# Optimization experiments

Hardware: AMD Instinct MI355X
Metric: run time of the kernel (lower is better)

The kernel has to match this reference:

```python
import jax, jax.numpy as jnp
import numpy as np
from jax import lax

T, B, D, H, L, NDIR = 512, 64, 512, 512, 3, 2

def _lengths():
    return 512 - 4 * np.arange(64)  # per-sequence lengths, non-increasing

def _qdq(w):
    # simulate dynamic int8 symmetric per-tensor weight quantization
    s = jnp.max(jnp.abs(w)) / 127.0
    return jnp.clip(jnp.round(w / s), -127, 127) * s

def setup_inputs() -> dict:
    key = jax.random.key(0)
    ks = jax.random.split(key, 9)
    lengths = _lengths()
    bs = np.array([(lengths > t).sum() for t in range(T)], dtype=np.int64)  # [T]
    pack_idx = np.concatenate([t * B + np.arange(bs[t]) for t in range(T)]).astype(np.int32)
    sc = 0.05
    data = jax.random.normal(ks[0], (int(bs.sum()), D), jnp.float32)
    h0 = jax.random.normal(ks[1], (L * NDIR, B, H), jnp.float32)
    c0 = jax.random.normal(ks[2], (L * NDIR, B, H), jnp.float32)
    w_ih0 = _qdq(jax.random.normal(ks[3], (NDIR, 4 * H, D)) * sc)
    w_hh0 = _qdq(jax.random.normal(ks[4], (NDIR, 4 * H, H)) * sc)
    b0 = jax.random.normal(ks[5], (NDIR, 4 * H)) * sc  # b_ih + b_hh combined
    w_ih_r = _qdq(jax.random.normal(ks[6], (L - 1, NDIR, 4 * H, NDIR * H)) * sc)
    w_hh_r = _qdq(jax.random.normal(ks[7], (L - 1, NDIR, 4 * H, H)) * sc)
    b_r = jax.random.normal(ks[8], (L - 1, NDIR, 4 * H)) * sc
    return {"data": data, "h0": h0, "c0": c0, "w_ih0": w_ih0, "w_hh0": w_hh0, "b0": b0,
            "w_ih_r": w_ih_r, "w_hh_r": w_hh_r, "b_r": b_r,
            "batch_sizes": jnp.asarray(bs), "pack_idx": jnp.asarray(pack_idx)}

def _run_dir(x, mask, h0, c0, w_ih, w_hh, b):
    # x: [T,B,in], mask: [T,B]; batch the input GEMM over all timesteps
    gx = jnp.einsum('tbd,gd->tbg', x, w_ih) + b  # [T,B,4H]
    def step(carry, inp):
        h, c = carry
        gx_t, m = inp
        gates = gx_t + h @ w_hh.T
        i, f, g, o = jnp.split(gates, 4, axis=-1)  # PyTorch gate order i,f,g,o
        c_new = jax.nn.sigmoid(f) * c + jax.nn.sigmoid(i) * jnp.tanh(g)
        h_new = jax.nn.sigmoid(o) * jnp.tanh(c_new)
        m = m[:, None]
        return (jnp.where(m, h_new, h), jnp.where(m, c_new, c)), jnp.where(m, h_new, h)
    (hT, cT), ys = lax.scan(step, (h0, c0), (gx, mask))
    return ys * mask[:, :, None], hT, cT

def _lstm(data, h0, c0, w_ih0, w_hh0, b0, w_ih_r, w_hh_r, b_r, batch_sizes, pack_idx):
    mask = jnp.arange(B)[None, :] < batch_sizes[:, None]          # [T,B] valid slots
    lengths = jnp.sum(mask, axis=0)                                # [B]
    rev_idx = jnp.clip(lengths[None, :] - 1 - jnp.arange(T)[:, None], 0, T - 1)  # [T,B]
    barange = jnp.arange(B)[None, :]
    x = jnp.zeros((T * B, D), data.dtype).at[pack_idx].set(data).reshape(T, B, D)
    h_ns, c_ns = [], []
    for l in range(L):
        outs = []
        for d in range(NDIR):
            if l == 0:
                w_ih, w_hh, b = w_ih0[d], w_hh0[d], b0[d]
            else:
                w_ih, w_hh, b = w_ih_r[l - 1, d], w_hh_r[l - 1, d], b_r[l - 1, d]
            hi, ci = h0[NDIR * l + d], c0[NDIR * l + d]
            if d == 0:
                ys, hT, cT = _run_dir(x, mask, hi, ci, w_ih, w_hh, b)
            else:
                x_rev = x[rev_idx, barange]               # per-sequence reversal
                ys_r, hT, cT = _run_dir(x_rev, mask, hi, ci, w_ih, w_hh, b)
                ys = ys_r[rev_idx, barange] * mask[:, :, None]
            outs.append(ys); h_ns.append(hT); c_ns.append(cT)
        x = jnp.concatenate(outs, axis=-1)  # [T,B,2H] feeds next layer
    out = x.reshape(T * B, NDIR * H)[pack_idx]  # repack to [total_tokens, 2H]
    return out, jnp.stack(h_ns), jnp.stack(c_ns)

def reference(data, h0, c0, w_ih0, w_hh0, b0, w_ih_r, w_hh_r, b_r, batch_sizes, pack_idx):
    return _lstm(data, h0, c0, w_ih0, w_hh0, b0, w_ih_r, w_hh_r, b_r, batch_sizes, pack_idx)
```

## Files before the change

kernel.cpp:

```cpp
#include <hip/hip_runtime.h>
#include <cmath>

typedef _Float16 f16;
typedef _Float16 half8 __attribute__((ext_vector_type(8)));
typedef float floatx4 __attribute__((ext_vector_type(4)));
typedef unsigned u32x4 __attribute__((ext_vector_type(4)));

#define NT 512
#define NB 64
#define NH 512
#define NG 2048
#define CHUNK 128

__device__ inline float sigf(float x) { return 1.0f / (1.0f + __expf(-x)); }
__device__ inline float tanhfast(float x) { return 2.0f / (1.0f + __expf(-2.0f * x)) - 1.0f; }

__device__ inline void load_lds16(const f16* g, f16* l) {
  __builtin_amdgcn_global_load_lds(
      (__attribute__((address_space(1))) void*)g,
      (__attribute__((address_space(3))) void*)l, 16, 0, 0);
}

__global__ void prep_meta(const int* __restrict__ bs_raw, int* __restrict__ lens,
                          int* __restrict__ cum) {
  __shared__ int sbs[NT];
  int stride = (bs_raw[1] == 0) ? 2 : 1;
  for (int i = threadIdx.x; i < NT; i += 256) sbs[i] = bs_raw[i * stride];
  __syncthreads();
  for (int b = threadIdx.x; b < NB; b += 256) {
    int n = 0;
    for (int t = 0; t < NT; ++t) n += (sbs[t] > b);
    lens[b] = n;
  }
  if (threadIdx.x == 0) {
    int run = 0;
    for (int t = 0; t < NT; ++t) { cum[t] = run; run += sbs[t]; }
  }
}

__global__ void scatter_rows(const float* __restrict__ data, const int* __restrict__ pidx,
                             f16* __restrict__ X0) {
  int r = blockIdx.x;
  int row = pidx[r];
  const float* src = data + (size_t)r * 512;
  f16* dst = X0 + (size_t)row * 512;
  for (int k = threadIdx.x; k < 512; k += 256) dst[k] = (f16)src[k];
}

__global__ void f32_to_f16(const float* __restrict__ in, f16* __restrict__ out, size_t n) {
  size_t i = (size_t)blockIdx.x * 256 + threadIdx.x;
  size_t stride = (size_t)gridDim.x * 256;
  for (; i < n; i += stride) out[i] = (f16)in[i];
}

__global__ void init_h(const float* __restrict__ h0, const float* __restrict__ c0,
                       float* __restrict__ hsave, float* __restrict__ csave,
                       unsigned* __restrict__ ht, unsigned* __restrict__ ctr, int layer) {
  int idx = blockIdx.x * 256 + threadIdx.x;
  int d = idx >> 15, rem = idx & 32767;
  float hv = h0[(size_t)(2 * layer + d) * NB * NH + rem];
  float cv = c0[(size_t)(2 * layer + d) * NB * NH + rem];
  hsave[idx] = hv;
  csave[idx] = cv;
  union { f16 f; unsigned short s; } hc; hc.f = (f16)hv;
  unsigned word = ((unsigned)(layer * NT) << 16) | hc.s;
  __hip_atomic_store(ht + (size_t)d * NB * NH + rem, word,
                     __ATOMIC_RELAXED, __HIP_MEMORY_SCOPE_AGENT);
  if (blockIdx.x == 0) {
    __hip_atomic_store(ctr + threadIdx.x, (unsigned)(layer * NT),
                       __ATOMIC_RELAXED, __HIP_MEMORY_SCOPE_AGENT);
  }
}

__global__ __launch_bounds__(256) void gemm_gx(const f16* __restrict__ A,
                                               const f16* __restrict__ W,
                                               const float* __restrict__ bias,
                                               const int* __restrict__ lens,
                                               f16* __restrict__ gxc, int K, int c0) {
  const int d = blockIdx.z;
  const int m0 = blockIdx.y * 128;
  const int n0 = blockIdx.x * 128;
  const f16* Wd = W + (size_t)d * NG * K;

  __shared__ __align__(16) f16 As[128 * 32];
  __shared__ __align__(16) f16 Bs[128 * 32];

  const int tid = threadIdx.x, lane = tid & 63, wv = tid >> 6;
  const int wm = wv >> 1, wn = wv & 1;
  const int lrow = lane >> 2, lcol = (lane & 3) * 8;
  const int q = lane >> 4, nn = lane & 15;

  const f16* aptr[2];
  const f16* bptr[2];
#pragma unroll
  for (int i = 0; i < 2; ++i) {
    int ch = wv * 2 + i;
    int m = m0 + ch * 16 + lrow;
    int t = c0 + (m >> 6), b = m & 63;
    int tt = t;
    if (d) { tt = lens[b] - 1 - t; tt = tt < 0 ? 0 : (tt > NT - 1 ? NT - 1 : tt); }
    aptr[i] = A + (size_t)(tt * NB + b) * K + lcol;
    bptr[i] = Wd + (size_t)(n0 + ch * 16 + lrow) * K + lcol;
  }

  floatx4 acc[4][4] = {};
  for (int k0 = 0; k0 < K; k0 += 32) {
    __syncthreads();
#pragma unroll
    for (int i = 0; i < 2; ++i) {
      int ch = wv * 2 + i;
      load_lds16(aptr[i] + k0, As + ch * 512);
      load_lds16(bptr[i] + k0, Bs + ch * 512);
    }
    __syncthreads();
    half8 a[4], b[4];
#pragma unroll
    for (int f = 0; f < 4; ++f) {
      a[f] = *(const half8*)(As + (wm * 64 + f * 16 + nn) * 32 + q * 8);
      b[f] = *(const half8*)(Bs + (wn * 64 + f * 16 + nn) * 32 + q * 8);
    }
#pragma unroll
    for (int fm = 0; fm < 4; ++fm)
#pragma unroll
      for (int fn = 0; fn < 4; ++fn)
        acc[fm][fn] = __builtin_amdgcn_mfma_f32_16x16x32_f16(a[fm], b[fn], acc[fm][fn], 0, 0, 0);
  }

  f16* gxd = gxc + (size_t)d * CHUNK * NB * NG;
#pragma unroll
  for (int fn = 0; fn < 4; ++fn) {
    int col = n0 + wn * 64 + fn * 16 + nn;
    float bv = bias[d * NG + col];
#pragma unroll
    for (int fm = 0; fm < 4; ++fm) {
      int mb = m0 + wm * 64 + fm * 16 + q * 4;
#pragma unroll
      for (int r = 0; r < 4; ++r)
        gxd[(size_t)(mb + r) * NG + col] = (f16)(acc[fm][fn][r] + bv);
    }
  }
}

__global__ __launch_bounds__(256, 1) void lstm_rec(
    const f16* __restrict__ gxc, const f16* __restrict__ whh,
    const int* __restrict__ lens, const int* __restrict__ cum,
    float* __restrict__ hsave, float* __restrict__ csave,
    unsigned* __restrict__ ht, unsigned* __restrict__ ctr,
    f16* __restrict__ Y, float* __restrict__ outp,
    float* __restrict__ hT, float* __restrict__ cT,
    int c0, int mode, int layer) {
  const int tid = threadIdx.x, lane = tid & 63, wv = tid >> 6;
  const int g = blockIdx.x & 7, w = blockIdx.x >> 3;
  const int dir = g & 1, bsl = g >> 1;
  const int q = lane >> 4, nn = lane & 15;

  const int maxlen = lens[bsl * 16];
  int nst = maxlen - c0;
  if (nst <= 0) return;
  if (nst > CHUNK) nst = CHUNK;

  __shared__ __align__(16) unsigned As[2][16][260];
  __shared__ float s_g[4][16][17];

  const int jbase = w * 16 + wv * 4;
  const int coln = (nn >> 2) * NH + jbase + (nn & 3);
  const f16* whd = whh + (size_t)dir * NG * NH;
  half8 bf[16];
#pragma unroll
  for (int s = 0; s < 16; ++s) {
    bf[s] = *(const half8*)(whd + (size_t)coln * NH + s * 32 + q * 8);
    asm volatile("" : "+v"(bf[s]));
  }

  const int b_e = bsl * 16 + nn;
  const int jglob = jbase + q;
  const int lene = lens[b_e];
  const int brow = bsl * 16 + q * 4;
  const int lidx = (dir * NB + b_e) * NH + jglob;
  float h = hsave[lidx], c = csave[lidx];

  const f16* gxd = gxc + (size_t)dir * CHUNK * NB * NG;
  const int ebase = layer * NT;

  const unsigned* cslot = ctr + (size_t)g * 32 + (lane & 31);

  for (int ct = 0; ct < nst; ++ct) {
    const int t = c0 + ct;
    const int e = ebase + t;
    const int par = t & 1;

    float gxv[4];
#pragma unroll
    for (int r = 0; r < 4; ++r)
      gxv[r] = (float)gxd[(size_t)(ct * NB + brow + r) * NG + coln];

    {
      const unsigned* cp = cslot + par * 256;
      int it = 0;
      for (;;) {
        unsigned cv = __hip_atomic_load(cp, __ATOMIC_RELAXED, __HIP_MEMORY_SCOPE_AGENT);
        if (__ballot((int)cv >= e) == ~0ull) break;
        if (++it > 200000) break;
        __builtin_amdgcn_s_sleep(1);
      }
    }

    const unsigned long long* p64 =
        (const unsigned long long*)(ht + ((size_t)(par * 2 + dir) * NB + bsl * 16 + nn) * NH +
                                    wv * 128 + q * 8);
    unsigned long long wb[16];
    {
      int it = 0;
      for (;;) {
#pragma unroll
        for (int i = 0; i < 16; ++i)
          wb[i] = __hip_atomic_load(p64 + (i >> 2) * 16 + (i & 3), __ATOMIC_RELAXED,
                                    __HIP_MEMORY_SCOPE_AGENT);
        unsigned tg = 0xffffu;
#pragma unroll
        for (int i = 0; i < 16; ++i) {
          tg &= (unsigned)(wb[i] >> 16) & 0xffffu;
          tg &= (unsigned)(wb[i] >> 48);
        }
        if (__ballot(tg >= (unsigned)e) == ~0ull) break;
        if (++it > 50000) break;
        __builtin_amdgcn_s_sleep(1);
      }
    }

#pragma unroll
    for (int s = 0; s < 4; ++s) {
      unsigned d0 = (unsigned)(wb[4 * s + 0] & 0xffffu) | ((unsigned)(wb[4 * s + 0] >> 32) << 16);
      unsigned d1 = (unsigned)(wb[4 * s + 1] & 0xffffu) | ((unsigned)(wb[4 * s + 1] >> 32) << 16);
      unsigned d2 = (unsigned)(wb[4 * s + 2] & 0xffffu) | ((unsigned)(wb[4 * s + 2] >> 32) << 16);
      unsigned d3 = (unsigned)(wb[4 * s + 3] & 0xffffu) | ((unsigned)(wb[4 * s + 3] >> 32) << 16);
      *(u32x4*)&As[par][nn][wv * 64 + s * 16 + q * 4] = (u32x4){d0, d1, d2, d3};
    }
    __syncthreads();

    floatx4 acc0 = {0.f, 0.f, 0.f, 0.f}, acc1 = {0.f, 0.f, 0.f, 0.f};
#pragma unroll
    for (int s = 0; s < 8; ++s) {
      half8 a0 = *(const half8*)&As[par][nn][(2 * s) * 16 + q * 4];
      half8 a1 = *(const half8*)&As[par][nn][(2 * s + 1) * 16 + q * 4];
      acc0 = __builtin_amdgcn_mfma_f32_16x16x32_f16(a0, bf[2 * s], acc0, 0, 0, 0);
      acc1 = __builtin_amdgcn_mfma_f32_16x16x32_f16(a1, bf[2 * s + 1], acc1, 0, 0, 0);
    }
#pragma unroll
    for (int r4 = 0; r4 < 4; ++r4) s_g[wv][q * 4 + r4][nn] = acc0[r4] + acc1[r4] + gxv[r4];

    const bool act = (t < lene);
    if (act) {
      float gi = s_g[wv][nn][q];
      float gf = s_g[wv][nn][4 + q];
      float gg = s_g[wv][nn][8 + q];
      float go = s_g[wv][nn][12 + q];
      c = sigf(gf) * c + sigf(gi) * tanhfast(gg);
      h = sigf(go) * tanhfast(c);
    }
    union { f16 f; unsigned short s; } hc; hc.f = (f16)h;
    unsigned word = ((unsigned)(e + 1) << 16) | hc.s;
    __hip_atomic_store(ht + ((size_t)(((t + 1) & 1) * 2 + dir) * NB + b_e) * NH + jglob,
                       word, __ATOMIC_RELAXED, __HIP_MEMORY_SCOPE_AGENT);
    if (tid == 0)
      __hip_atomic_store(ctr + (size_t)(((t + 1) & 1) * 256 + g * 32 + w), (unsigned)(e + 1),
                         __ATOMIC_RELAXED, __HIP_MEMORY_SCOPE_AGENT);
    if (mode == 0) {
      int tp = act ? (dir ? (lene - 1 - t) : t) : t;
      Y[(size_t)(tp * NB + b_e) * (2 * NH) + dir * NH + jglob] = act ? (f16)h : (f16)0.f;
    } else if (act) {
      int tp = dir ? (lene - 1 - t) : t;
      outp[(size_t)(cum[tp] + b_e) * (2 * NH) + dir * NH + jglob] = h;
    }
  }

  hsave[lidx] = h;
  csave[lidx] = c;
  const int sidx = ((2 * layer + dir) * NB + b_e) * NH + jglob;
  hT[sidx] = h;
  cT[sidx] = c;
}

extern "C" void kernel_launch(void* const* d_in, const int* in_sizes, int n_in,
                              void* d_out, int out_size, void* d_ws, size_t ws_size,
                              hipStream_t stream) {
  const float* data  = (const float*)d_in[0];
  const float* h0    = (const float*)d_in[1];
  const float* c0    = (const float*)d_in[2];
  const float* w_ih0 = (const float*)d_in[3];
  const float* w_hh0 = (const float*)d_in[4];
  const float* b0    = (const float*)d_in[5];
  const float* w_ihr = (const float*)d_in[6];
  const float* w_hhr = (const float*)d_in[7];
  const float* b_r   = (const float*)d_in[8];
  const int* bs_raw  = (const int*)d_in[9];
  const int* pidx    = (const int*)d_in[10];
  const int nrows = in_sizes[0] / 512;
  float* out = (float*)d_out;

  f16* Y0 = (f16*)d_out;
  float* hT = out + (size_t)nrows * 1024;
  float* cT = hT + (size_t)6 * NB * NH;

  char* p = (char*)d_ws;
  auto take = [&](size_t bytes) {
    char* r = p;
    p += (bytes + 255) & ~(size_t)255;
    return (void*)r;
  };
  f16* gxc   = (f16*)take((size_t)2 * CHUNK * NB * NG * 2);
  f16* Y1    = (f16*)take((size_t)NT * NB * 1024 * 2);
  f16* X0    = Y1;
  f16* wih16 = (f16*)take((size_t)2 * NG * 1024 * 2);
  f16* whh16 = (f16*)take((size_t)2 * NG * NH * 2);
  unsigned* ht = (unsigned*)take((size_t)2 * 2 * NB * NH * 4);
  unsigned* ctr = (unsigned*)take((size_t)2 * 8 * 32 * 4);
  float* hsave = (float*)take((size_t)2 * NB * NH * 4);
  float* csave = (float*)take((size_t)2 * NB * NH * 4);
  int* lens = (int*)take(256);
  int* cum  = (int*)take(NT * 4);

  prep_meta<<<1, 256, 0, stream>>>(bs_raw, lens, cum);
  (void)hipMemsetAsync(X0, 0, (size_t)NT * NB * 512 * 2, stream);
  (void)hipMemsetAsync(ht, 0, (size_t)2 * 2 * NB * NH * 4, stream);
  (void)hipMemsetAsync(ctr, 0, (size_t)2 * 8 * 32 * 4, stream);
  scatter_rows<<<nrows, 256, 0, stream>>>(data, pidx, X0);

  for (int l = 0; l < 3; ++l) {
    const float* wih_f = (l == 0) ? w_ih0 : w_ihr + (size_t)(l - 1) * 2 * NG * 1024;
    const float* whh_f = (l == 0) ? w_hh0 : w_hhr + (size_t)(l - 1) * 2 * NG * NH;
    const float* bias  = (l == 0) ? b0 : b_r + (size_t)(l - 1) * 2 * NG;
    const int K = (l == 0) ? 512 : 1024;
    const f16* Xl = (l == 0) ? X0 : ((l == 1) ? Y0 : Y1);
    f16* Yl = (l == 0) ? Y0 : Y1;
    f32_to_f16<<<256, 256, 0, stream>>>(wih_f, wih16, (size_t)2 * NG * K);
    f32_to_f16<<<256, 256, 0, stream>>>(whh_f, whh16, (size_t)2 * NG * NH);
    init_h<<<256, 256, 0, stream>>>(h0, c0, hsave, csave, ht, ctr, l);
    for (int c = 0; c < 4; ++c) {
      gemm_gx<<<dim3(16, 64, 2), 256, 0, stream>>>(Xl, wih16, bias, lens, gxc, K, c * CHUNK);
      lstm_rec<<<256, 256, 0, stream>>>(gxc, whh16, lens, cum, hsave, csave, ht, ctr, Yl,
                                        out, hT, cT, c * CHUNK, (l == 2) ? 1 : 0, l);
    }
  }
}
```

Baseline: 7.056 ms.

## Overlap next-chunk input GEMM with recurrent kernel via double-buffered gate buffers

Extracts the input-projection GEMM into a device function and launches it inside the recurrent kernel as extra blocks (index 256 and up), computing the next chunk's gate pre-activations into a second buffer while the current chunk's recurrence runs. Double buffering is enabled only when the workspace has room for the second buffer. This hides the separate GEMM launches behind the latency-bound recurrence. The risk is that the extra blocks compete with the persistent recurrent blocks for CUs and bandwidth, or delay their scheduling, since those blocks spin-wait on each other.

```diff
diff --git a/kernel.cpp b/kernel.cpp
--- a/kernel.cpp
+++ b/kernel.cpp
@@ -72,14 +72,12 @@
   }
 }
 
-__global__ __launch_bounds__(256) void gemm_gx(const f16* __restrict__ A,
-                                               const f16* __restrict__ W,
-                                               const float* __restrict__ bias,
-                                               const int* __restrict__ lens,
-                                               f16* __restrict__ gxc, int K, int c0) {
-  const int d = blockIdx.z;
-  const int m0 = blockIdx.y * 128;
-  const int n0 = blockIdx.x * 128;
+__device__ void gemm_body(const f16* __restrict__ A, const f16* __restrict__ W,
+                          const float* __restrict__ bias, const int* __restrict__ lens,
+                          f16* __restrict__ gxc, int K, int c0, int id) {
+  const int d = id >> 10;
+  const int m0 = ((id >> 4) & 63) * 128;
+  const int n0 = (id & 15) * 128;
   const f16* Wd = W + (size_t)d * NG * K;
 
   __shared__ __align__(16) f16 As[128 * 32];
@@ -141,6 +139,15 @@
   }
 }
 
+__global__ __launch_bounds__(256) void gemm_gx(const f16* __restrict__ A,
+                                               const f16* __restrict__ W,
+                                               const float* __restrict__ bias,
+                                               const int* __restrict__ lens,
+                                               f16* __restrict__ gxc, int K, int c0) {
+  gemm_body(A, W, bias, lens, gxc, K, c0,
+            (int)(blockIdx.z * 1024 + blockIdx.y * 16 + blockIdx.x));
+}
+
 __global__ __launch_bounds__(256, 1) void lstm_rec(
     const f16* __restrict__ gxc, const f16* __restrict__ whh,
     const int* __restrict__ lens, const int* __restrict__ cum,
@@ -148,7 +155,13 @@
     unsigned* __restrict__ ht, unsigned* __restrict__ ctr,
     f16* __restrict__ Y, float* __restrict__ outp,
     float* __restrict__ hT, float* __restrict__ cT,
-    int c0, int mode, int layer) {
+    int c0, int mode, int layer,
+    const f16* __restrict__ Xg, const f16* __restrict__ wih,
+    const float* __restrict__ biasg, f16* __restrict__ gxn, int Kg, int c0n) {
+  if (blockIdx.x >= 256) {
+    if (gxn) gemm_body(Xg, wih, biasg, lens, gxn, Kg, c0n, (int)blockIdx.x - 256);
+    return;
+  }
   const int tid = threadIdx.x, lane = tid & 63, wv = tid >> 6;
   const int g = blockIdx.x & 7, w = blockIdx.x >> 3;
   const int dir = g & 1, bsl = g >> 1;
@@ -308,7 +321,8 @@
     p += (bytes + 255) & ~(size_t)255;
     return (void*)r;
   };
-  f16* gxc   = (f16*)take((size_t)2 * CHUNK * NB * NG * 2);
+  const size_t gsz = (size_t)2 * CHUNK * NB * NG * 2;
+  f16* gxcA  = (f16*)take(gsz);
   f16* Y1    = (f16*)take((size_t)NT * NB * 1024 * 2);
   f16* X0    = Y1;
   f16* wih16 = (f16*)take((size_t)2 * NG * 1024 * 2);
@@ -319,6 +333,9 @@
   float* csave = (float*)take((size_t)2 * NB * NH * 4);
   int* lens = (int*)take(256);
   int* cum  = (int*)take(NT * 4);
+  f16* gxcB = nullptr;
+  if ((size_t)(p - (char*)d_ws) + gsz <= ws_size) gxcB = (f16*)take(gsz);
+  const bool fuse = (gxcB != nullptr);
 
   prep_meta<<<1, 256, 0, stream>>>(bs_raw, lens, cum);
   (void)hipMemsetAsync(X0, 0, (size_t)NT * NB * 512 * 2, stream);
@@ -337,9 +354,15 @@
     f32_to_f16<<<256, 256, 0, stream>>>(whh_f, whh16, (size_t)2 * NG * NH);
     init_h<<<256, 256, 0, stream>>>(h0, c0, hsave, csave, ht, ctr, l);
     for (int c = 0; c < 4; ++c) {
-      gemm_gx<<<dim3(16, 64, 2), 256, 0, stream>>>(Xl, wih16, bias, lens, gxc, K, c * CHUNK);
-      lstm_rec<<<256, 256, 0, stream>>>(gxc, whh16, lens, cum, hsave, csave, ht, ctr, Yl,
-                                        out, hT, cT, c * CHUNK, (l == 2) ? 1 : 0, l);
-    }
-  }
-}
+      f16* gcur = fuse ? ((c & 1) ? gxcB : gxcA) : gxcA;
+      if (c == 0 || !fuse)
+        gemm_gx<<<dim3(16, 64, 2), 256, 0, stream>>>(Xl, wih16, bias, lens, gcur, K, c * CHUNK);
+      const bool g_on = fuse && (c < 3);
+      f16* gnext = g_on ? (((c + 1) & 1) ? gxcB : gxcA) : nullptr;
+      const int grid = g_on ? 2304 : 256;
+      lstm_rec<<<grid, 256, 0, stream>>>(gcur, whh16, lens, cum, hsave, csave, ht, ctr, Yl,
+                                         out, hT, cT, c * CHUNK, (l == 2) ? 1 : 0, l,
+                                         Xl, wih16, bias, gnext, K, (c + 1) * CHUNK);
+    }
+  }
+}
```

Result: no change. 6.990 ms (-0.9%).
